# Kernel optimization log

Measured on AMD Instinct MI355X. Metric: run time of the kernel, lower is better.

Reference implementation:

```python
import jax, jax.numpy as jnp
import numpy as np

C = 64          # residual channels
N_LAYERS = 30
MAX_STEPS = 200
SQRT2 = 2.0 ** 0.5


def _conv1d(x, W, b, dilation=1, pad=0):
    # x: [B, Cin, T], W: [Cout, Cin, K], b: [Cout]
    y = jax.lax.conv_general_dilated(
        x, W, window_strides=(1,), padding=[(pad, pad)],
        rhs_dilation=(dilation,), dimension_numbers=('NCH', 'OIH', 'NCH'))
    return y + b[None, :, None]


def _silu(x):
    return x * jax.nn.sigmoid(x)


def _emb_table():
    steps = jnp.arange(MAX_STEPS, dtype=jnp.float32)[:, None]      # [200,1]
    dims = jnp.arange(64, dtype=jnp.float32)[None, :]              # [1,64]
    t = steps * 10.0 ** (dims * 4.0 / 63.0)                        # [200,64]
    return jnp.concatenate([jnp.sin(t), jnp.cos(t)], axis=1)       # [200,128]


def setup_inputs() -> dict:
    key = jax.random.key(0)
    ks = jax.random.split(key, 20)
    B, T = 4, 16384
    f32 = jnp.float32
    inp = {
        'audio': jax.random.normal(ks[0], (B, 1, T), dtype=f32),
        'diffusion_step': jax.random.randint(ks[1], (B,), 0, MAX_STEPS),
        # input projection Conv1d(1, 64, 1)
        'in_W': jax.random.normal(ks[2], (C, 1, 1), f32) * 1.0,
        'in_b': jax.random.normal(ks[3], (C,), f32) * 0.01,
        # diffusion embedding MLP 128->512->512
        'p1_W': jax.random.normal(ks[4], (512, 128), f32) * (1.0 / np.sqrt(128)),
        'p1_b': jnp.zeros((512,), f32),
        'p2_W': jax.random.normal(ks[5], (512, 512), f32) * (1.0 / np.sqrt(512)),
        'p2_b': jnp.zeros((512,), f32),
        # per-layer params (stacked over 30 layers)
        'dw_W': jax.random.normal(ks[6], (N_LAYERS, 2 * C, C, 3), f32) * (1.0 / np.sqrt(3 * C)),
        'dw_b': jnp.zeros((N_LAYERS, 2 * C), f32),
        'dp_W': jax.random.normal(ks[7], (N_LAYERS, C, 512), f32) * (1.0 / np.sqrt(512)),
        'dp_b': jnp.zeros((N_LAYERS, C), f32),
        'op_W': jax.random.normal(ks[8], (N_LAYERS, 2 * C, C, 1), f32) * (1.0 / np.sqrt(C)),
        'op_b': jnp.zeros((N_LAYERS, 2 * C), f32),
        # skip projection Conv1d(64,64,1)
        'sk_W': jax.random.normal(ks[9], (C, C, 1), f32) * (1.0 / np.sqrt(C)),
        'sk_b': jnp.zeros((C,), f32),
        # output projection Conv1d(64,1,1), weight zero-init like original
        'out_W': jnp.zeros((1, C, 1), f32),
        'out_b': jax.random.normal(ks[10], (1,), f32) * 0.01,
    }
    return inp


def reference(audio, diffusion_step, in_W, in_b, p1_W, p1_b, p2_W, p2_b,
              dw_W, dw_b, dp_W, dp_b, op_W, op_b, sk_W, sk_b, out_W, out_b):
    x = jax.nn.relu(_conv1d(audio, in_W, in_b))                    # [B,64,T]
    # diffusion embedding
    t = _emb_table()[diffusion_step]                               # [B,128]
    t = _silu(t @ p1_W.T + p1_b)                                   # [B,512]
    t = _silu(t @ p2_W.T + p2_b)                                   # [B,512]
    skip = None
    for i in range(N_LAYERS):
        d = 2 ** (i % 10)
        cond = (t @ dp_W[i].T + dp_b[i])[:, :, None]               # [B,64,1]
        y = _conv1d(x + cond, dw_W[i], dw_b[i], dilation=d, pad=d) # [B,128,T]
        gate, filt = y[:, :C], y[:, C:]
        y = jax.nn.sigmoid(gate) * jnp.tanh(filt)                  # [B,64,T]
        y = _conv1d(y, op_W[i], op_b[i])                           # [B,128,T]
        residual, sk = y[:, :C], y[:, C:]
        x = (x + residual) / SQRT2
        skip = sk if skip is None else skip + sk
    x = skip / np.sqrt(float(N_LAYERS)).astype(np.float32)
    x = jax.nn.relu(_conv1d(x, sk_W, sk_b))
    return _conv1d(x, out_W, out_b)                                # [B,1,T]
```

## Files before the change

kernel.cpp:

```cpp
#include <hip/hip_runtime.h>
#include <math.h>

#define C 64
#define NL 30
#define T 16384
#define B 4

typedef __bf16 bf16_t;
typedef __bf16 bf16x8 __attribute__((ext_vector_type(8)));
typedef __bf16 bf16x4 __attribute__((ext_vector_type(4)));
typedef float f32x4 __attribute__((ext_vector_type(4)));

typedef const __attribute__((address_space(1))) unsigned int glb_u32;
typedef __attribute__((address_space(3))) unsigned int lds_u32;

constexpr float INV_SQRT2   = 0.70710678118654752440f;
constexpr float INV_SQRT_NL = 0.18257418583505537115f;

__device__ __forceinline__ float fsig(float x) {
    return __builtin_amdgcn_rcpf(1.f + __builtin_amdgcn_exp2f(-1.44269504089f * x));
}
__device__ __forceinline__ float ftanh(float x) {
    return fmaf(2.f, __builtin_amdgcn_rcpf(1.f + __builtin_amdgcn_exp2f(-2.88539008178f * x)), -1.f);
}
// ... 37 lines not shown
    __syncthreads();
    int ol = tid >> 2, q = tid & 3;
    int o = blk * 64 + ol;
    const float4* wr = (const float4*)(p1_W + o * 128 + q * 32);
    const float4* ev = (const float4*)(e + q * 32);
    float a = 0.f;
    #pragma unroll
    for (int j = 0; j < 8; ++j) {
        float4 wv = wr[j]; float4 xv = ev[j];
        a = fmaf(wv.x, xv.x, a); a = fmaf(wv.y, xv.y, a);
        a = fmaf(wv.z, xv.z, a); a = fmaf(wv.w, xv.w, a);
    }
    red[tid] = a;
    __syncthreads();
    if (q == 0) {
        float v = red[tid] + red[tid + 1] + red[tid + 2] + red[tid + 3] + p1_b[o];
        h1out[b * 512 + o] = v / (1.f + expf(-v));
    }
}

__global__ void cond_p2(const float* __restrict__ h1,
                        const float* __restrict__ p2_W, const float* __restrict__ p2_b,
                        float* __restrict__ h2out) {
    __shared__ float red[256];
    int b = blockIdx.x, blk = blockIdx.y, tid = threadIdx.x;
    int ol = tid >> 2, q = tid & 3;
    int o = blk * 64 + ol;
    const float4* wr = (const float4*)(p2_W + o * 512 + q * 128);
    const float4* hv = (const float4*)(h1 + b * 512 + q * 128);
    float a = 0.f;
    #pragma unroll 8
    for (int j = 0; j < 32; ++j) {
        float4 wv = wr[j]; float4 xv = hv[j];
        a = fmaf(wv.x, xv.x, a); a = fmaf(wv.y, xv.y, a);
        a = fmaf(wv.z, xv.z, a); a = fmaf(wv.w, xv.w, a);
    }
    red[tid] = a;
    __syncthreads();
    if (q == 0) {
        float v = red[tid] + red[tid + 1] + red[tid + 2] + red[tid + 3] + p2_b[o];
        h2out[b * 512 + o] = v / (1.f + expf(-v));
    }
}

__global__ void cond_stage2b(const float* __restrict__ h2,
                             const float* __restrict__ dp_W, const float* __restrict__ dp_b,
                             const bf16_t* __restrict__ convpk,
                             const float* __restrict__ dw_b,
                             float* __restrict__ bias2) {
    __shared__ float red[256];
    __shared__ float cond_s[64];
    int l = blockIdx.x, b = blockIdx.y;
    int tid = threadIdx.x;
    {
        int o = tid >> 2, q = tid & 3;
        const float4* wr = (const float4*)(dp_W + ((size_t)l * C + o) * 512 + q * 128);
        const float4* h = (const float4*)(h2 + b * 512 + q * 128);
        float a = 0.f;
        #pragma unroll 8
        for (int j = 0; j < 32; ++j) {
            float4 wv = wr[j]; float4 hv = h[j];
            a = fmaf(wv.x, hv.x, a); a = fmaf(wv.y, hv.y, a);
            a = fmaf(wv.z, hv.z, a); a = fmaf(wv.w, hv.w, a);
        }
        red[tid] = a;
        __syncthreads();
        if (q == 0)
            cond_s[o] = red[tid] + red[tid + 1] + red[tid + 2] + red[tid + 3] + dp_b[l * C + o];
    }
    __syncthreads();
    int oc = tid & 127, kh = tid >> 7;
    const bf16_t* wr = convpk + ((size_t)l * 128 + oc) * 192 + kh * 96;
    float a = kh ? 0.f : dw_b[l * 128 + oc];
    #pragma unroll
    for (int j = 0; j < 96; ++j)
        a = fmaf((float)wr[j], cond_s[(kh * 96 + j) & 63], a);
    __syncthreads();
    red[tid] = a;
    __syncthreads();
    if (tid < 128)
        bias2[(l * B + b) * 128 + tid] = red[tid] + red[tid + 128];
}

__global__ __launch_bounds__(256, 4) void layer_kernel(
    const bf16_t* __restrict__ x_in, bf16_t* __restrict__ x_out, bf16_t* __restrict__ skip,
    const bf16_t* __restrict__ convpk, const bf16_t* __restrict__ oppk,
    const float* __restrict__ bias2, const float* __restrict__ op_b,
    const bf16_t* __restrict__ zpage,
    int layer, int dil, int first)
{
    __shared__ uint4 smem_u[2048];
    char* sm = (char*)smem_u;

    int tid = threadIdx.x;
    int w = __builtin_amdgcn_readfirstlane(tid >> 6);
    int l = tid & 63;
    int lr = l & 15;
    int g = l >> 4;
    int b = blockIdx.y;
    int bid = blockIdx.x;
    int tile = ((bid & 7) << 5) + (bid >> 3);
    int t0 = tile * 64;
    const bf16_t* xb = x_in + (size_t)b * T * 64;
    size_t bb = (size_t)b * T * 64;

    #pragma unroll
    for (int it = 0; it < 6; ++it) {
        int qq = it * 256 + tid;
        int slice = qq >> 9, row = (qq >> 3) & 63, c16 = qq & 7;
        int ts = t0 + row + (slice - 1) * dil;
        int c16s = c16 ^ (row & 7);
        const bf16_t* src = ((unsigned)ts < (unsigned)T)
            ? (xb + (size_t)ts * 64 + c16s * 8)
            : (zpage + c16s * 8);
        __builtin_amdgcn_global_load_lds((glb_u32*)src,
            (lds_u32*)(sm + it * 4096 + w * 1024), 16, 0, 0);
    }

    bf16x8 cA[2][6];
    const bf16_t* cw = convpk + (size_t)layer * 128 * 192;
    #pragma unroll
    for (int mf = 0; mf < 2; ++mf)
        #pragma unroll
        for (int kf = 0; kf < 6; ++kf)
            cA[mf][kf] = *(const bf16x8*)(cw + (mf * 64 + w * 16 + lr) * 192 + kf * 32 + g * 8);
    f32x4 bC[2];
    const float* b2 = bias2 + (layer * B + b) * 128;
    #pragma unroll
    for (int mf = 0; mf < 2; ++mf)
        #pragma unroll
        for (int r = 0; r < 4; ++r) bC[mf][r] = b2[mf * 64 + w * 16 + g * 4 + r];
    __syncthreads();

    f32x4 acc[2][4];
    #pragma unroll
    for (int mf = 0; mf < 2; ++mf)
        #pragma unroll
        for (int nf = 0; nf < 4; ++nf) acc[mf][nf] = bC[mf];
    #pragma unroll
    for (int kf = 0; kf < 6; ++kf) {
        int tap = kf >> 1;
        int kc = (kf & 1) * 32;
        bf16x8 Bf[4];
        #pragma unroll
        for (int nf = 0; nf < 4; ++nf) {
            int off = tap * 8192 + (nf * 16 + lr) * 128 + (kc + g * 8) * 2;
            Bf[nf] = *(const bf16x8*)(sm + swz(off));
        }
        #pragma unroll
        for (int mf = 0; mf < 2; ++mf)
            #pragma unroll
            for (int nf = 0; nf < 4; ++nf)
                acc[mf][nf] = __builtin_amdgcn_mfma_f32_16x16x32_bf16(
                    cA[mf][kf], Bf[nf], acc[mf][nf], 0, 0, 0);
    }

    bf16x8 oA[2][2];
    const bf16_t* ow = oppk + (size_t)layer * 128 * 64;
    #pragma unroll
    for (int mf = 0; mf < 2; ++mf)
        #pragma unroll
        for (int kf = 0; kf < 2; ++kf)
            oA[mf][kf] = *(const bf16x8*)(ow + (mf * 64 + w * 16 + lr) * 64 + kf * 32 + g * 8);
    f32x4 bO[2];
    const float* ob = op_b + layer * 2 * C;
    #pragma unroll
    for (int mf = 0; mf < 2; ++mf)
        #pragma unroll
        for (int r = 0; r < 4; ++r) bO[mf][r] = ob[mf * 64 + w * 16 + g * 4 + r];

    #pragma unroll
    for (int nf = 0; nf < 4; ++nf) {
        union { bf16_t hh[4]; uint2 u; } zp;
        #pragma unroll
        for (int r = 0; r < 4; ++r)
            zp.hh[r] = (bf16_t)(fsig(acc[0][nf][r]) * ftanh(acc[1][nf][r]));
        int off = 24576 + (nf * 16 + lr) * 128 + (w * 16 + g * 4) * 2;
        *(uint2*)(sm + swz(off)) = zp.u;
    }
    __syncthreads();

    f32x4 acc2[2][4];
    #pragma unroll
    for (int mf = 0; mf < 2; ++mf)
        #pragma unroll
        for (int nf = 0; nf < 4; ++nf) acc2[mf][nf] = bO[mf];
    #pragma unroll
    for (int kf = 0; kf < 2; ++kf) {
        bf16x8 Zf[4];
        #pragma unroll
        for (int nf = 0; nf < 4; ++nf) {
            int off = 24576 + (nf * 16 + lr) * 128 + (kf * 32 + g * 8) * 2;
            Zf[nf] = *(const bf16x8*)(sm + swz(off));
        }
        #pragma unroll
        for (int mf = 0; mf < 2; ++mf)
            #pragma unroll
            for (int nf = 0; nf < 4; ++nf)
                acc2[mf][nf] = __builtin_amdgcn_mfma_f32_16x16x32_bf16(
                    oA[mf][kf], Zf[nf], acc2[mf][nf], 0, 0, 0);
    }

    #pragma unroll
    for (int nf = 0; nf < 4; ++nf) {
        int t = t0 + nf * 16 + lr;
        int c0 = w * 16 + g * 4;
        int xoff = 8192 + (nf * 16 + lr) * 128 + c0 * 2;
        bf16x4 xv = *(const bf16x4*)(sm + swz(xoff));
        bf16x4 ro, so;
        bf16_t* sp = skip + bb + (size_t)t * 64 + c0;
        if (first) {
            #pragma unroll
            for (int r = 0; r < 4; ++r) {
                ro[r] = (bf16_t)(((float)xv[r] + acc2[0][nf][r]) * INV_SQRT2);
                so[r] = (bf16_t)acc2[1][nf][r];
            }
        } else {
            bf16x4 sv = *(const bf16x4*)sp;
            #pragma unroll
            for (int r = 0; r < 4; ++r) {
                ro[r] = (bf16_t)(((float)xv[r] + acc2[0][nf][r]) * INV_SQRT2);
                so[r] = (bf16_t)((float)sv[r] + acc2[1][nf][r]);
            }
        }
        *(bf16x4*)(x_out + bb + (size_t)t * 64 + c0) = ro;
        *(bf16x4*)sp = so;
    }
}

template<int D1, int D2, int YOFF, int NYR, int XOFF, int NXR, int FROMAUD>
__global__ __launch_bounds__(256) void fused_pair(
    const bf16_t* __restrict__ x_in, bf16_t* __restrict__ x_out,
    bf16_t* __restrict__ skip,
    const bf16_t* __restrict__ convpk, const bf16_t* __restrict__ oppk,
    const float* __restrict__ bias2, const float* __restrict__ op_b,
    const bf16_t* __restrict__ zpage,
    const float* __restrict__ audio,
    const float* __restrict__ in_W, const float* __restrict__ in_b,
    int layerA, int first)
{
    extern __shared__ char sm[];
    constexpr int NYF = NYR / 16;
    constexpr int CF  = YOFF / 16;
    constexpr int YS  = NXR * 128;
    constexpr int ZS  = YS + NYR * 128;

    int tid = threadIdx.x;
    int w = __builtin_amdgcn_readfirstlane(tid >> 6);
    int l = tid & 63, lr = l & 15, g = l >> 4;
    int bid = blockIdx.x;
    int tile = ((bid & 7) << 5) + (bid >> 3);
    int b = blockIdx.y;
    int t0 = tile * 64;
    size_t bb = (size_t)b * T * 64;
    const bf16_t* xb = x_in + bb;
    int c0 = w * 16 + g * 4;

    if constexpr (FROMAUD) {
        #pragma unroll
        for (int r = 0; r < NXR / 32; ++r) {
            int q = r * 256 + tid;
            int row = q >> 3, c16 = q & 7;
            int ts = t0 - XOFF + row;
            bf16x8 o;
            if ((unsigned)ts < (unsigned)T) {
                float av = audio[(size_t)b * T + ts];
                #pragma unroll
                for (int j = 0; j < 8; ++j) {
                    int c = c16 * 8 + j;
                    o[j] = (bf16_t)fmaxf(fmaf(in_W[c], av, in_b[c]), 0.f);
                }
            } else {
                #pragma unroll
                for (int j = 0; j < 8; ++j) o[j] = (bf16_t)0.f;
            }
            *(bf16x8*)(sm + swz(row * 128 + c16 * 16)) = o;
        }
    } else {
        #pragma unroll
        for (int r = 0; r < NXR / 32; ++r) {
            int row = r * 32 + (tid >> 3), c16 = tid & 7;
            int ts = t0 - XOFF + row;
            int c16s = c16 ^ (row & 7);
            const bf16_t* src = ((unsigned)ts < (unsigned)T)
                ? (xb + (size_t)ts * 64 + c16s * 8)
                : (zpage + c16s * 8);
            __builtin_amdgcn_global_load_lds((glb_u32*)src,
                (lds_u32*)(sm + r * 4096 + w * 1024), 16, 0, 0);
        }
    }

    float skr[16];
    #pragma unroll
    for (int i = 0; i < 16; ++i) skr[i] = 0.f;

    bf16x8 cA[2][6];
    {
        const bf16_t* cw = convpk + (size_t)layerA * 128 * 192;
        #pragma unroll
        for (int mf = 0; mf < 2; ++mf)
            #pragma unroll
            for (int kf = 0; kf < 6; ++kf)
                cA[mf][kf] = *(const bf16x8*)(cw + (mf * 64 + w * 16 + lr) * 192 + kf * 32 + g * 8);
    }
    bf16x8 oA[2][2];
    {
        const bf16_t* ow = oppk + (size_t)layerA * 128 * 64;
        #pragma unroll
        for (int mf = 0; mf < 2; ++mf)
            #pragma unroll
            for (int kf = 0; kf < 2; ++kf)
                oA[mf][kf] = *(const bf16x8*)(ow + (mf * 64 + w * 16 + lr) * 64 + kf * 32 + g * 8);
    }
    f32x4 bC[2], bO[2];
    {
        const float* b2 = bias2 + (layerA * B + b) * 128;
        const float* ob = op_b + layerA * 2 * C;
        #pragma unroll
        for (int mf = 0; mf < 2; ++mf)
            #pragma unroll
            for (int r = 0; r < 4; ++r) {
                bC[mf][r] = b2[mf * 64 + c0 + r];
                bO[mf][r] = ob[mf * 64 + c0 + r];
            }
    }
    __syncthreads();

    f32x4 acc[2][NYF];
    #pragma unroll
    for (int mf = 0; mf < 2; ++mf)
        #pragma unroll
        for (int nf = 0; nf < NYF; ++nf) acc[mf][nf] = bC[mf];
    #pragma unroll
    for (int kf = 0; kf < 6; ++kf) {
        int tap = kf >> 1;
        int kc = (kf & 1) * 32;
        bf16x8 Bf[NYF];
        #pragma unroll
        for (int nf = 0; nf < NYF; ++nf) {
            int ix = (nf * 16 + lr) + (XOFF - YOFF) + (tap - 1) * D1;
            Bf[nf] = *(const bf16x8*)(sm + swz(ix * 128 + (kc + g * 8) * 2));
        }
        #pragma unroll
        for (int mf = 0; mf < 2; ++mf)
            #pragma unroll
            for (int nf = 0; nf < NYF; ++nf)
                acc[mf][nf] = __builtin_amdgcn_mfma_f32_16x16x32_bf16(
                    cA[mf][kf], Bf[nf], acc[mf][nf], 0, 0, 0);
    }

    #pragma unroll
    for (int nf = 0; nf < NYF; ++nf) {
        union { bf16_t hh[4]; uint2 u; } zp;
        #pragma unroll
        for (int r = 0; r < 4; ++r)
            zp.hh[r] = (bf16_t)(fsig(acc[0][nf][r]) * ftanh(acc[1][nf][r]));
        int off = ZS + (nf * 16 + lr) * 128 + c0 * 2;
        *(uint2*)(sm + swz(off)) = zp.u;
    }
    __syncthreads();

    {
        f32x4 acc2[2][NYF];
        #pragma unroll
        for (int mf = 0; mf < 2; ++mf)
            #pragma unroll
            for (int nf = 0; nf < NYF; ++nf) acc2[mf][nf] = bO[mf];
        #pragma unroll
        for (int kf = 0; kf < 2; ++kf) {
            bf16x8 Zf[NYF];
            #pragma unroll
            for (int nf = 0; nf < NYF; ++nf) {
                int off = ZS + (nf * 16 + lr) * 128 + (kf * 32 + g * 8) * 2;
                Zf[nf] = *(const bf16x8*)(sm + swz(off));
            }
            #pragma unroll
            for (int mf = 0; mf < 2; ++mf)
                #pragma unroll
                for (int nf = 0; nf < NYF; ++nf)
                    acc2[mf][nf] = __builtin_amdgcn_mfma_f32_16x16x32_bf16(
                        oA[mf][kf], Zf[nf], acc2[mf][nf], 0, 0, 0);
        }
        #pragma unroll
        for (int nf = 0; nf < NYF; ++nf) {
            int iy = nf * 16 + lr;
            int ta = t0 - YOFF + iy;
            bool inr = ((unsigned)ta < (unsigned)T);
            int ixc = iy + (XOFF - YOFF);
            bf16x4 xv = *(const bf16x4*)(sm + swz(ixc * 128 + c0 * 2));
            bf16x4 yo;
            #pragma unroll
            for (int r = 0; r < 4; ++r) {
                float yv = ((float)xv[r] + acc2[0][nf][r]) * INV_SQRT2;
                yo[r] = inr ? (bf16_t)yv : (bf16_t)0.f;
                if (nf >= CF && nf < CF + 4)
                    skr[(nf - CF) * 4 + r] += acc2[1][nf][r];
            }
            *(bf16x4*)(sm + swz(YS + iy * 128 + c0 * 2)) = yo;
        }
    }

    int layerB = layerA + 1;
    bf16x8 cB[2][6];
    {
        const bf16_t* cw = convpk + (size_t)layerB * 128 * 192;
        #pragma unroll
        for (int mf = 0; mf < 2; ++mf)
            #pragma unroll
            for (int kf = 0; kf < 6; ++kf)
                cB[mf][kf] = *(const bf16x8*)(cw + (mf * 64 + w * 16 + lr) * 192 + kf * 32 + g * 8);
    }
    bf16x8 oB[2][2];
    {
        const bf16_t* ow = oppk + (size_t)layerB * 128 * 64;
        #pragma unroll
        for (int mf = 0; mf < 2; ++mf)
            #pragma unroll
            for (int kf = 0; kf < 2; ++kf)
                oB[mf][kf] = *(const bf16x8*)(ow + (mf * 64 + w * 16 + lr) * 64 + kf * 32 + g * 8);
    }
    f32x4 bCB[2], bOB[2];
    {
        const float* b2 = bias2 + (layerB * B + b) * 128;
        const float* ob = op_b + layerB * 2 * C;
        #pragma unroll
        for (int mf = 0; mf < 2; ++mf)
            #pragma unroll
            for (int r = 0; r < 4; ++r) {
                bCB[mf][r] = b2[mf * 64 + c0 + r];
                bOB[mf][r] = ob[mf * 64 + c0 + r];
            }
    }
    __syncthreads();

    f32x4 accB[2][4];
    #pragma unroll
    for (int mf = 0; mf < 2; ++mf)
        #pragma unroll
        for (int nf = 0; nf < 4; ++nf) accB[mf][nf] = bCB[mf];
    #pragma unroll
    for (int kf = 0; kf < 6; ++kf) {
        int tap = kf >> 1;
        int kc = (kf & 1) * 32;
        bf16x8 Bf[4];
        #pragma unroll
        for (int nf = 0; nf < 4; ++nf) {
            int jy = (nf * 16 + lr) + YOFF + (tap - 1) * D2;
            Bf[nf] = *(const bf16x8*)(sm + swz(YS + jy * 128 + (kc + g * 8) * 2));
        }
        #pragma unroll
        for (int mf = 0; mf < 2; ++mf)
            #pragma unroll
            for (int nf = 0; nf < 4; ++nf)
                accB[mf][nf] = __builtin_amdgcn_mfma_f32_16x16x32_bf16(
                    cB[mf][kf], Bf[nf], accB[mf][nf], 0, 0, 0);
    }

    #pragma unroll
    for (int nf = 0; nf < 4; ++nf) {
        union { bf16_t hh[4]; uint2 u; } zp;
        #pragma unroll
        for (int r = 0; r < 4; ++r)
            zp.hh[r] = (bf16_t)(fsig(accB[0][nf][r]) * ftanh(accB[1][nf][r]));
        int off = ZS + (nf * 16 + lr) * 128 + c0 * 2;
        *(uint2*)(sm + swz(off)) = zp.u;
    }
    __syncthreads();

    f32x4 acc2B[2][4];
    #pragma unroll
    for (int mf = 0; mf < 2; ++mf)
        #pragma unroll
        for (int nf = 0; nf < 4; ++nf) acc2B[mf][nf] = bOB[mf];
    #pragma unroll
    for (int kf = 0; kf < 2; ++kf) {
        bf16x8 Zf[4];
        #pragma unroll
        for (int nf = 0; nf < 4; ++nf) {
            int off = ZS + (nf * 16 + lr) * 128 + (kf * 32 + g * 8) * 2;
            Zf[nf] = *(const bf16x8*)(sm + swz(off));
        }
        #pragma unroll
        for (int mf = 0; mf < 2; ++mf)
            #pragma unroll
            for (int nf = 0; nf < 4; ++nf)
                acc2B[mf][nf] = __builtin_amdgcn_mfma_f32_16x16x32_bf16(
                    oB[mf][kf], Zf[nf], acc2B[mf][nf], 0, 0, 0);
    }
    #pragma unroll
    for (int nf = 0; nf < 4; ++nf) {
        int it = nf * 16 + lr;
        int t = t0 + it;
        int jyc = it + YOFF;
        bf16x4 yv = *(const bf16x4*)(sm + swz(YS + jyc * 128 + c0 * 2));
        bf16x4 ro, so;
        bf16_t* sp = skip + bb + (size_t)t * 64 + c0;
        if (first) {
            #pragma unroll
            for (int r = 0; r < 4; ++r) {
                ro[r] = (bf16_t)(((float)yv[r] + acc2B[0][nf][r]) * INV_SQRT2);
                so[r] = (bf16_t)(skr[nf * 4 + r] + acc2B[1][nf][r]);
            }
        } else {
            bf16x4 sv = *(const bf16x4*)sp;
            #pragma unroll
            for (int r = 0; r < 4; ++r) {
                ro[r] = (bf16_t)(((float)yv[r] + acc2B[0][nf][r]) * INV_SQRT2);
                so[r] = (bf16_t)((float)sv[r] + skr[nf * 4 + r] + acc2B[1][nf][r]);
            }
        }
        *(bf16x4*)(x_out + bb + (size_t)t * 64 + c0) = ro;
        *(bf16x4*)sp = so;
    }
}

__global__ __launch_bounds__(256) void final_kernel(
    const bf16_t* __restrict__ skip, const bf16_t* __restrict__ skpk,
    const float* __restrict__ sk_b,
    const float* __restrict__ out_W, const float* __restrict__ out_b,
    float* __restrict__ out)
{
    __shared__ uint4 tile_u[512];
    __shared__ float part[16][66];
    unsigned char* sm = (unsigned char*)tile_u;
    int tid = threadIdx.x;
    int w = __builtin_amdgcn_readfirstlane(tid >> 6);
    int l = tid & 63, lr = l & 15, g = l >> 4;
    int bid = blockIdx.x;
    int tile = ((bid & 7) << 5) + (bid >> 3);
    int b = blockIdx.y, t0 = tile * 64;
    const bf16_t* sb = skip + (size_t)b * T * 64;

    #pragma unroll
    for (int it = 0; it < 2; ++it) {
        int q = it * 256 + tid;
        int row = q >> 3, c16 = q & 7;
        uint4 val = *(const uint4*)(sb + (size_t)(t0 + row) * 64 + c16 * 8);
        *(uint4*)(sm + swz(row * 128 + c16 * 16)) = val;
    }

    bf16x8 aS[2];
    #pragma unroll
    for (int kf = 0; kf < 2; ++kf)
        aS[kf] = *(const bf16x8*)(skpk + (w * 16 + lr) * 64 + kf * 32 + g * 8);
    f32x4 acc[4];
    #pragma unroll
    for (int nf = 0; nf < 4; ++nf)
        #pragma unroll
        for (int r = 0; r < 4; ++r) acc[nf][r] = sk_b[w * 16 + g * 4 + r];
    __syncthreads();

    #pragma unroll
    for (int kf = 0; kf < 2; ++kf) {
        bf16x8 Bf[4];
        #pragma unroll
        for (int nf = 0; nf < 4; ++nf) {
            int off = (nf * 16 + lr) * 128 + (kf * 32 + g * 8) * 2;
            Bf[nf] = *(const bf16x8*)(sm + swz(off));
        }
        #pragma unroll
        for (int nf = 0; nf < 4; ++nf)
            acc[nf] = __builtin_amdgcn_mfma_f32_16x16x32_bf16(aS[kf], Bf[nf], acc[nf], 0, 0, 0);
    }

    #pragma unroll
    for (int nf = 0; nf < 4; ++nf) {
        float o = 0.f;
        #pragma unroll
        for (int r = 0; r < 4; ++r)
            o = fmaf(out_W[w * 16 + g * 4 + r], fmaxf(acc[nf][r], 0.f), o);
        part[w * 4 + g][nf * 16 + lr] = o;
    }
    __syncthreads();
    if (tid < 64) {
        float o = out_b[0];
        #pragma unroll
        for (int j = 0; j < 16; ++j) o += part[j][tid];
        out[(size_t)b * T + t0 + tid] = o;
    }
}

extern "C" void kernel_launch(void* const* d_in, const int* in_sizes, int n_in,
                              void* d_out, int out_size, void* d_ws, size_t ws_size,
                              hipStream_t stream) {
    const float* audio = (const float*)d_in[0];
    const int*   dstep = (const int*)d_in[1];
    const float* in_W  = (const float*)d_in[2];
    const float* in_b  = (const float*)d_in[3];
    const float* p1_W  = (const float*)d_in[4];
    const float* p1_b  = (const float*)d_in[5];
    const float* p2_W  = (const float*)d_in[6];
    const float* p2_b  = (const float*)d_in[7];
    const float* dw_W  = (const float*)d_in[8];
    const float* dw_b  = (const float*)d_in[9];
    const float* dp_W  = (const float*)d_in[10];
    const float* dp_b  = (const float*)d_in[11];
    const float* op_W  = (const float*)d_in[12];
    const float* op_b  = (const float*)d_in[13];
    const float* sk_W  = (const float*)d_in[14];
    const float* sk_b  = (const float*)d_in[15];
    const float* out_W = (const float*)d_in[16];
    const float* out_b = (const float*)d_in[17];

    float* ws = (float*)d_ws;
    const size_t NXE = (size_t)B * T * 64;
    float* h1    = ws;
    float* h2    = h1 + B * 512;
    float* bias2 = h2 + B * 512;
    float* zpg   = bias2 + NL * B * 128;
    bf16_t* xA   = (bf16_t*)(zpg + 128);
    bf16_t* xB   = xA + NXE;
    bf16_t* skip = xB + NXE;
    bf16_t* convpk = skip + NXE;
    bf16_t* oppk   = convpk + (size_t)NL * 128 * 192;
    bf16_t* skpk   = oppk + (size_t)NL * 128 * 64;

    hipMemsetAsync(zpg, 0, 512, stream);
    hipLaunchKernelGGL(pack_weights, dim3(3856), dim3(256), 0, stream,
                       dw_W, op_W, sk_W, convpk, oppk, skpk);
    hipLaunchKernelGGL(cond_embp1, dim3(B, 8), dim3(256), 0, stream,
                       dstep, p1_W, p1_b, h1);
    hipLaunchKernelGGL(cond_p2, dim3(B, 8), dim3(256), 0, stream,
                       h1, p2_W, p2_b, h2);
    hipLaunchKernelGGL(cond_stage2b, dim3(NL, B), dim3(256), 0, stream,
                       h2, dp_W, dp_b, convpk, dw_b, bias2);

    bf16_t* bufs[2] = { xA, xB };
    int cur = 0;
    const bf16_t* zpgc = (const bf16_t*)zpg;
    for (int dec = 0; dec < 3; ++dec) {
        int base = dec * 10;
        if (dec == 0) {
            hipLaunchKernelGGL((fused_pair<1, 2, 16, 96, 32, 128, 1>),
                               dim3(T / 64, B), dim3(256), 40960, stream,
                               bufs[cur], bufs[cur ^ 1], skip, convpk, oppk,
                               bias2, op_b, zpgc, audio, in_W, in_b, 0, 1);
        } else {
            hipLaunchKernelGGL((fused_pair<1, 2, 16, 96, 32, 128, 0>),
                               dim3(T / 64, B), dim3(256), 40960, stream,
                               bufs[cur], bufs[cur ^ 1], skip, convpk, oppk,
                               bias2, op_b, zpgc, audio, in_W, in_b, base + 0, 0);
        }
        cur ^= 1;
        hipLaunchKernelGGL((fused_pair<4, 8, 16, 96, 32, 128, 0>),
                           dim3(T / 64, B), dim3(256), 40960, stream,
                           bufs[cur], bufs[cur ^ 1], skip, convpk, oppk,
                           bias2, op_b, zpgc, audio, in_W, in_b, base + 2, 0);
        cur ^= 1;
        hipLaunchKernelGGL((fused_pair<16, 32, 32, 128, 48, 160, 0>),
                           dim3(T / 64, B), dim3(256), 53248, stream,
                           bufs[cur], bufs[cur ^ 1], skip, convpk, oppk,
                           bias2, op_b, zpgc, audio, in_W, in_b, base + 4, 0);
        cur ^= 1;
        for (int j = 6; j < 10; ++j) {
            int dil = 1 << j;
            hipLaunchKernelGGL(layer_kernel, dim3(T / 64, B), dim3(256), 0, stream,
                               bufs[cur], bufs[cur ^ 1], skip, convpk, oppk,
                               bias2, op_b, zpgc, base + j, dil, 0);
            cur ^= 1;
        }
    }
    hipLaunchKernelGGL(final_kernel, dim3(T / 64, B), dim3(256), 0, stream,
                       skip, skpk, sk_b, out_W, out_b, (float*)d_out);
}
```

Before: 484.9 us.

## Fuse three dilated layers per kernel and process two tiles per block in layer_kernel

Result: slower. 519.2 us (+7.1%).

```diff
diff --git a/kernel.cpp b/kernel.cpp
--- a/kernel.cpp
+++ b/kernel.cpp
@@ -143,7 +143,7 @@
         bias2[(l * B + b) * 128 + tid] = red[tid] + red[tid + 128];
 }
 
-__global__ __launch_bounds__(256, 4) void layer_kernel(
+__global__ __launch_bounds__(256) void layer_kernel(
     const bf16_t* __restrict__ x_in, bf16_t* __restrict__ x_out, bf16_t* __restrict__ skip,
     const bf16_t* __restrict__ convpk, const bf16_t* __restrict__ oppk,
     const float* __restrict__ bias2, const float* __restrict__ op_b,
@@ -160,23 +160,9 @@
     int g = l >> 4;
     int b = blockIdx.y;
     int bid = blockIdx.x;
-    int tile = ((bid & 7) << 5) + (bid >> 3);
-    int t0 = tile * 64;
+    int tile = ((bid & 7) << 4) + (bid >> 3);
+    int tbase = tile * 128;
     const bf16_t* xb = x_in + (size_t)b * T * 64;
-    size_t bb = (size_t)b * T * 64;
-
-    #pragma unroll
-    for (int it = 0; it < 6; ++it) {
-        int qq = it * 256 + tid;
-        int slice = qq >> 9, row = (qq >> 3) & 63, c16 = qq & 7;
-        int ts = t0 + row + (slice - 1) * dil;
-        int c16s = c16 ^ (row & 7);
-        const bf16_t* src = ((unsigned)ts < (unsigned)T)
-            ? (xb + (size_t)ts * 64 + c16s * 8)
-            : (zpage + c16s * 8);
-        __builtin_amdgcn_global_load_lds((glb_u32*)src,
-            (lds_u32*)(sm + it * 4096 + w * 1024), 16, 0, 0);
-    }
 
     bf16x8 cA[2][6];
     const bf16_t* cw = convpk + (size_t)layer * 128 * 192;
@@ -185,37 +171,6 @@
         #pragma unroll
         for (int kf = 0; kf < 6; ++kf)
             cA[mf][kf] = *(const bf16x8*)(cw + (mf * 64 + w * 16 + lr) * 192 + kf * 32 + g * 8);
-    f32x4 bC[2];
-    const float* b2 = bias2 + (layer * B + b) * 128;
-    #pragma unroll
-    for (int mf = 0; mf < 2; ++mf)
-        #pragma unroll
-        for (int r = 0; r < 4; ++r) bC[mf][r] = b2[mf * 64 + w * 16 + g * 4 + r];
-    __syncthreads();
-
-    f32x4 acc[2][4];
-    #pragma unroll
-    for (int mf = 0; mf < 2; ++mf)
-        #pragma unroll
-        for (int nf = 0; nf < 4; ++nf) acc[mf][nf] = bC[mf];
-    #pragma unroll
-    for (int kf = 0; kf < 6; ++kf) {
-        int tap = kf >> 1;
-        int kc = (kf & 1) * 32;
-        bf16x8 Bf[4];
-        #pragma unroll
-        for (int nf = 0; nf < 4; ++nf) {
-            int off = tap * 8192 + (nf * 16 + lr) * 128 + (kc + g * 8) * 2;
-            Bf[nf] = *(const bf16x8*)(sm + swz(off));
-        }
-        #pragma unroll
-        for (int mf = 0; mf < 2; ++mf)
-            #pragma unroll
-            for (int nf = 0; nf < 4; ++nf)
-                acc[mf][nf] = __builtin_amdgcn_mfma_f32_16x16x32_bf16(
-                    cA[mf][kf], Bf[nf], acc[mf][nf], 0, 0, 0);
-    }
-
     bf16x8 oA[2][2];
     const bf16_t* ow = oppk + (size_t)layer * 128 * 64;
     #pragma unroll
@@ -223,74 +178,123 @@
         #pragma unroll
         for (int kf = 0; kf < 2; ++kf)
             oA[mf][kf] = *(const bf16x8*)(ow + (mf * 64 + w * 16 + lr) * 64 + kf * 32 + g * 8);
-    f32x4 bO[2];
+    f32x4 bC[2], bO[2];
+    const float* b2 = bias2 + (layer * B + b) * 128;
     const float* ob = op_b + layer * 2 * C;
     #pragma unroll
     for (int mf = 0; mf < 2; ++mf)
         #pragma unroll
-        for (int r = 0; r < 4; ++r) bO[mf][r] = ob[mf * 64 + w * 16 + g * 4 + r];
-
-    #pragma unroll
-    for (int nf = 0; nf < 4; ++nf) {
-        union { bf16_t hh[4]; uint2 u; } zp;
-        #pragma unroll
-        for (int r = 0; r < 4; ++r)
-            zp.hh[r] = (bf16_t)(fsig(acc[0][nf][r]) * ftanh(acc[1][nf][r]));
-        int off = 24576 + (nf * 16 + lr) * 128 + (w * 16 + g * 4) * 2;
-        *(uint2*)(sm + swz(off)) = zp.u;
-    }
-    __syncthreads();
-
-    f32x4 acc2[2][4];
-    #pragma unroll
-    for (int mf = 0; mf < 2; ++mf)
-        #pragma unroll
-        for (int nf = 0; nf < 4; ++nf) acc2[mf][nf] = bO[mf];
-    #pragma unroll
-    for (int kf = 0; kf < 2; ++kf) {
-        bf16x8 Zf[4];
+        for (int r = 0; r < 4; ++r) {
+            bC[mf][r] = b2[mf * 64 + w * 16 + g * 4 + r];
+            bO[mf][r] = ob[mf * 64 + w * 16 + g * 4 + r];
+        }
+
+    size_t bb = (size_t)b * T * 64;
+
+    for (int st = 0; st < 2; ++st) {
+        int t0 = tbase + st * 64;
+
+        #pragma unroll
+        for (int it = 0; it < 6; ++it) {
+            int qq = it * 256 + tid;
+            int slice = qq >> 9, row = (qq >> 3) & 63, c16 = qq & 7;
+            int ts = t0 + row + (slice - 1) * dil;
+            int c16s = c16 ^ (row & 7);
+            const bf16_t* src = ((unsigned)ts < (unsigned)T)
+                ? (xb + (size_t)ts * 64 + c16s * 8)
+                : (zpage + c16s * 8);
+            __builtin_amdgcn_global_load_lds((glb_u32*)src,
+                (lds_u32*)(sm + it * 4096 + w * 1024), 16, 0, 0);
+        }
+        __syncthreads();
+
+        f32x4 acc[2][4];
+        #pragma unroll
+        for (int mf = 0; mf < 2; ++mf)
+            #pragma unroll
+            for (int nf = 0; nf < 4; ++nf) acc[mf][nf] = bC[mf];
+        #pragma unroll
+        for (int kf = 0; kf < 6; ++kf) {
+            int tap = kf >> 1;
+            int kc = (kf & 1) * 32;
+            bf16x8 Bf[4];
+            #pragma unroll
+            for (int nf = 0; nf < 4; ++nf) {
+                int off = tap * 8192 + (nf * 16 + lr) * 128 + (kc + g * 8) * 2;
+                Bf[nf] = *(const bf16x8*)(sm + swz(off));
+            }
+            #pragma unroll
+            for (int mf = 0; mf < 2; ++mf)
+                #pragma unroll
+                for (int nf = 0; nf < 4; ++nf)
+                    acc[mf][nf] = __builtin_amdgcn_mfma_f32_16x16x32_bf16(
+                        cA[mf][kf], Bf[nf], acc[mf][nf], 0, 0, 0);
+        }
+
         #pragma unroll
         for (int nf = 0; nf < 4; ++nf) {
-            int off = 24576 + (nf * 16 + lr) * 128 + (kf * 32 + g * 8) * 2;
-            Zf[nf] = *(const bf16x8*)(sm + swz(off));
-        }
+            union { bf16_t hh[4]; uint2 u; } zp;
+            #pragma unroll
+            for (int r = 0; r < 4; ++r)
+                zp.hh[r] = (bf16_t)(fsig(acc[0][nf][r]) * ftanh(acc[1][nf][r]));
+            int off = 24576 + (nf * 16 + lr) * 128 + (w * 16 + g * 4) * 2;
+            *(uint2*)(sm + swz(off)) = zp.u;
+        }
+        __syncthreads();
+
+        f32x4 acc2[2][4];
         #pragma unroll
         for (int mf = 0; mf < 2; ++mf)
             #pragma unroll
-            for (int nf = 0; nf < 4; ++nf)
-                acc2[mf][nf] = __builtin_amdgcn_mfma_f32_16x16x32_bf16(
-                    oA[mf][kf], Zf[nf], acc2[mf][nf], 0, 0, 0);
-    }
-
-    #pragma unroll
-    for (int nf = 0; nf < 4; ++nf) {
-        int t = t0 + nf * 16 + lr;
-        int c0 = w * 16 + g * 4;
-        int xoff = 8192 + (nf * 16 + lr) * 128 + c0 * 2;
-        bf16x4 xv = *(const bf16x4*)(sm + swz(xoff));
-        bf16x4 ro, so;
-        bf16_t* sp = skip + bb + (size_t)t * 64 + c0;
-        if (first) {
-            #pragma unroll
-            for (int r = 0; r < 4; ++r) {
-                ro[r] = (bf16_t)(((float)xv[r] + acc2[0][nf][r]) * INV_SQRT2);
-                so[r] = (bf16_t)acc2[1][nf][r];
-            }
-        } else {
-            bf16x4 sv = *(const bf16x4*)sp;
-            #pragma unroll
-            for (int r = 0; r < 4; ++r) {
-                ro[r] = (bf16_t)(((float)xv[r] + acc2[0][nf][r]) * INV_SQRT2);
-                so[r] = (bf16_t)((float)sv[r] + acc2[1][nf][r]);
-            }
-        }
-        *(bf16x4*)(x_out + bb + (size_t)t * 64 + c0) = ro;
-        *(bf16x4*)sp = so;
-    }
-}
-
-template<int D1, int D2, int YOFF, int NYR, int XOFF, int NXR, int FROMAUD>
-__global__ __launch_bounds__(256) void fused_pair(
+            for (int nf = 0; nf < 4; ++nf) acc2[mf][nf] = bO[mf];
+        #pragma unroll
+        for (int kf = 0; kf < 2; ++kf) {
+            bf16x8 Zf[4];
+            #pragma unroll
+            for (int nf = 0; nf < 4; ++nf) {
+                int off = 24576 + (nf * 16 + lr) * 128 + (kf * 32 + g * 8) * 2;
+                Zf[nf] = *(const bf16x8*)(sm + swz(off));
+            }
+            #pragma unroll
+            for (int mf = 0; mf < 2; ++mf)
+                #pragma unroll
+                for (int nf = 0; nf < 4; ++nf)
+                    acc2[mf][nf] = __builtin_amdgcn_mfma_f32_16x16x32_bf16(
+                        oA[mf][kf], Zf[nf], acc2[mf][nf], 0, 0, 0);
+        }
+
+        #pragma unroll
+        for (int nf = 0; nf < 4; ++nf) {
+            int t = t0 + nf * 16 + lr;
+            int c0 = w * 16 + g * 4;
+            int xoff = 8192 + (nf * 16 + lr) * 128 + c0 * 2;
+            bf16x4 xv = *(const bf16x4*)(sm + swz(xoff));
+            bf16x4 ro, so;
+            bf16_t* sp = skip + bb + (size_t)t * 64 + c0;
+            if (first) {
+                #pragma unroll
+                for (int r = 0; r < 4; ++r) {
+                    ro[r] = (bf16_t)(((float)xv[r] + acc2[0][nf][r]) * INV_SQRT2);
+                    so[r] = (bf16_t)acc2[1][nf][r];
+                }
+            } else {
+                bf16x4 sv = *(const bf16x4*)sp;
+                #pragma unroll
+                for (int r = 0; r < 4; ++r) {
+                    ro[r] = (bf16_t)(((float)xv[r] + acc2[0][nf][r]) * INV_SQRT2);
+                    so[r] = (bf16_t)((float)sv[r] + acc2[1][nf][r]);
+                }
+            }
+            *(bf16x4*)(x_out + bb + (size_t)t * 64 + c0) = ro;
+            *(bf16x4*)sp = so;
+        }
+        if (st == 0) __syncthreads();
+    }
+}
+
+template<int D1, int D2, int D3, int YB, int NYB, int YA, int NYA,
+         int XO, int NXR, int FROMAUD>
+__global__ __launch_bounds__(256) void fused_triple(
     const bf16_t* __restrict__ x_in, bf16_t* __restrict__ x_out,
     bf16_t* __restrict__ skip,
     const bf16_t* __restrict__ convpk, const bf16_t* __restrict__ oppk,
@@ -301,10 +305,12 @@
     int layerA, int first)
 {
     extern __shared__ char sm[];
-    constexpr int NYF = NYR / 16;
-    constexpr int CF  = YOFF / 16;
+    constexpr int NAF = NYA / 16;
+    constexpr int NBF = NYB / 16;
+    constexpr int CFA = YA / 16;
+    constexpr int CFB = YB / 16;
     constexpr int YS  = NXR * 128;
-    constexpr int ZS  = YS + NYR * 128;
+    constexpr int ZS  = YS + NYA * 128;
 
     int tid = threadIdx.x;
     int w = __builtin_amdgcn_readfirstlane(tid >> 6);
@@ -322,7 +328,7 @@
         for (int r = 0; r < NXR / 32; ++r) {
             int q = r * 256 + tid;
             int row = q >> 3, c16 = q & 7;
-            int ts = t0 - XOFF + row;
+            int ts = t0 - XO + row;
             bf16x8 o;
             if ((unsigned)ts < (unsigned)T) {
                 float av = audio[(size_t)b * T + ts];
@@ -341,7 +347,7 @@
         #pragma unroll
         for (int r = 0; r < NXR / 32; ++r) {
             int row = r * 32 + (tid >> 3), c16 = tid & 7;
-            int ts = t0 - XOFF + row;
+            int ts = t0 - XO + row;
             int c16s = c16 ^ (row & 7);
             const bf16_t* src = ((unsigned)ts < (unsigned)T)
                 ? (xb + (size_t)ts * 64 + c16s * 8)
@@ -355,223 +361,296 @@
     #pragma unroll
     for (int i = 0; i < 16; ++i) skr[i] = 0.f;
 
-    bf16x8 cA[2][6];
+    bf16x8 cW[2][6], oW[2][2];
+    f32x4 bC[2], bO[2];
     {
         const bf16_t* cw = convpk + (size_t)layerA * 128 * 192;
-        #pragma unroll
-        for (int mf = 0; mf < 2; ++mf)
-            #pragma unroll
-            for (int kf = 0; kf < 6; ++kf)
-                cA[mf][kf] = *(const bf16x8*)(cw + (mf * 64 + w * 16 + lr) * 192 + kf * 32 + g * 8);
-    }
-    bf16x8 oA[2][2];
-    {
         const bf16_t* ow = oppk + (size_t)layerA * 128 * 64;
-        #pragma unroll
-        for (int mf = 0; mf < 2; ++mf)
-            #pragma unroll
-            for (int kf = 0; kf < 2; ++kf)
-                oA[mf][kf] = *(const bf16x8*)(ow + (mf * 64 + w * 16 + lr) * 64 + kf * 32 + g * 8);
-    }
-    f32x4 bC[2], bO[2];
-    {
         const float* b2 = bias2 + (layerA * B + b) * 128;
         const float* ob = op_b + layerA * 2 * C;
         #pragma unroll
-        for (int mf = 0; mf < 2; ++mf)
+        for (int mf = 0; mf < 2; ++mf) {
+            #pragma unroll
+            for (int kf = 0; kf < 6; ++kf)
+                cW[mf][kf] = *(const bf16x8*)(cw + (mf * 64 + w * 16 + lr) * 192 + kf * 32 + g * 8);
+            #pragma unroll
+            for (int kf = 0; kf < 2; ++kf)
+                oW[mf][kf] = *(const bf16x8*)(ow + (mf * 64 + w * 16 + lr) * 64 + kf * 32 + g * 8);
             #pragma unroll
             for (int r = 0; r < 4; ++r) {
                 bC[mf][r] = b2[mf * 64 + c0 + r];
                 bO[mf][r] = ob[mf * 64 + c0 + r];
             }
-    }
-    __syncthreads();
-
-    f32x4 acc[2][NYF];
-    #pragma unroll
-    for (int mf = 0; mf < 2; ++mf)
-        #pragma unroll
-        for (int nf = 0; nf < NYF; ++nf) acc[mf][nf] = bC[mf];
-    #pragma unroll
-    for (int kf = 0; kf < 6; ++kf) {
-        int tap = kf >> 1;
-        int kc = (kf & 1) * 32;
-        bf16x8 Bf[NYF];
-        #pragma unroll
-        for (int nf = 0; nf < NYF; ++nf) {
-            int ix = (nf * 16 + lr) + (XOFF - YOFF) + (tap - 1) * D1;
-            Bf[nf] = *(const bf16x8*)(sm + swz(ix * 128 + (kc + g * 8) * 2));
-        }
+        }
+    }
+    __syncthreads();
+
+    {
+        f32x4 acc[2][NAF];
         #pragma unroll
         for (int mf = 0; mf < 2; ++mf)
             #pragma unroll
-            for (int nf = 0; nf < NYF; ++nf)
-                acc[mf][nf] = __builtin_amdgcn_mfma_f32_16x16x32_bf16(
-                    cA[mf][kf], Bf[nf], acc[mf][nf], 0, 0, 0);
-    }
-
-    #pragma unroll
-    for (int nf = 0; nf < NYF; ++nf) {
-        union { bf16_t hh[4]; uint2 u; } zp;
-        #pragma unroll
-        for (int r = 0; r < 4; ++r)
-            zp.hh[r] = (bf16_t)(fsig(acc[0][nf][r]) * ftanh(acc[1][nf][r]));
-        int off = ZS + (nf * 16 + lr) * 128 + c0 * 2;
-        *(uint2*)(sm + swz(off)) = zp.u;
-    }
-    __syncthreads();
-
-    {
-        f32x4 acc2[2][NYF];
+            for (int nf = 0; nf < NAF; ++nf) acc[mf][nf] = bC[mf];
+        #pragma unroll
+        for (int kf = 0; kf < 6; ++kf) {
+            int tap = kf >> 1;
+            int kc = (kf & 1) * 32;
+            bf16x8 Bf[NAF];
+            #pragma unroll
+            for (int nf = 0; nf < NAF; ++nf) {
+                int ix = (nf * 16 + lr) + (XO - YA) + (tap - 1) * D1;
+                Bf[nf] = *(const bf16x8*)(sm + swz(ix * 128 + (kc + g * 8) * 2));
+            }
+            #pragma unroll
+            for (int mf = 0; mf < 2; ++mf)
+                #pragma unroll
+                for (int nf = 0; nf < NAF; ++nf)
+                    acc[mf][nf] = __builtin_amdgcn_mfma_f32_16x16x32_bf16(
+                        cW[mf][kf], Bf[nf], acc[mf][nf], 0, 0, 0);
+        }
+        #pragma unroll
+        for (int nf = 0; nf < NAF; ++nf) {
+            union { bf16_t hh[4]; uint2 u; } zp;
+            #pragma unroll
+            for (int r = 0; r < 4; ++r)
+                zp.hh[r] = (bf16_t)(fsig(acc[0][nf][r]) * ftanh(acc[1][nf][r]));
+            *(uint2*)(sm + swz(ZS + (nf * 16 + lr) * 128 + c0 * 2)) = zp.u;
+        }
+    }
+    __syncthreads();
+
+    {
+        f32x4 acc2[2][NAF];
         #pragma unroll
         for (int mf = 0; mf < 2; ++mf)
             #pragma unroll
-            for (int nf = 0; nf < NYF; ++nf) acc2[mf][nf] = bO[mf];
+            for (int nf = 0; nf < NAF; ++nf) acc2[mf][nf] = bO[mf];
         #pragma unroll
         for (int kf = 0; kf < 2; ++kf) {
-            bf16x8 Zf[NYF];
-            #pragma unroll
-            for (int nf = 0; nf < NYF; ++nf) {
-                int off = ZS + (nf * 16 + lr) * 128 + (kf * 32 + g * 8) * 2;
-                Zf[nf] = *(const bf16x8*)(sm + swz(off));
-            }
+            bf16x8 Zf[NAF];
+            #pragma unroll
+            for (int nf = 0; nf < NAF; ++nf)
+                Zf[nf] = *(const bf16x8*)(sm + swz(ZS + (nf * 16 + lr) * 128 + (kf * 32 + g * 8) * 2));
             #pragma unroll
             for (int mf = 0; mf < 2; ++mf)
                 #pragma unroll
-                for (int nf = 0; nf < NYF; ++nf)
+                for (int nf = 0; nf < NAF; ++nf)
                     acc2[mf][nf] = __builtin_amdgcn_mfma_f32_16x16x32_bf16(
-                        oA[mf][kf], Zf[nf], acc2[mf][nf], 0, 0, 0);
-        }
-        #pragma unroll
-        for (int nf = 0; nf < NYF; ++nf) {
+                        oW[mf][kf], Zf[nf], acc2[mf][nf], 0, 0, 0);
+        }
+        #pragma unroll
+        for (int nf = 0; nf < NAF; ++nf) {
             int iy = nf * 16 + lr;
-            int ta = t0 - YOFF + iy;
+            int ta = t0 - YA + iy;
             bool inr = ((unsigned)ta < (unsigned)T);
-            int ixc = iy + (XOFF - YOFF);
+            int ixc = iy + (XO - YA);
             bf16x4 xv = *(const bf16x4*)(sm + swz(ixc * 128 + c0 * 2));
             bf16x4 yo;
             #pragma unroll
             for (int r = 0; r < 4; ++r) {
                 float yv = ((float)xv[r] + acc2[0][nf][r]) * INV_SQRT2;
                 yo[r] = inr ? (bf16_t)yv : (bf16_t)0.f;
-                if (nf >= CF && nf < CF + 4)
-                    skr[(nf - CF) * 4 + r] += acc2[1][nf][r];
+                if (nf >= CFA && nf < CFA + 4)
+                    skr[(nf - CFA) * 4 + r] += acc2[1][nf][r];
             }
             *(bf16x4*)(sm + swz(YS + iy * 128 + c0 * 2)) = yo;
         }
     }
-
-    int layerB = layerA + 1;
-    bf16x8 cB[2][6];
-    {
+    {
+        int layerB = layerA + 1;
         const bf16_t* cw = convpk + (size_t)layerB * 128 * 192;
-        #pragma unroll
-        for (int mf = 0; mf < 2; ++mf)
-            #pragma unroll
-            for (int kf = 0; kf < 6; ++kf)
-                cB[mf][kf] = *(const bf16x8*)(cw + (mf * 64 + w * 16 + lr) * 192 + kf * 32 + g * 8);
-    }
-    bf16x8 oB[2][2];
-    {
         const bf16_t* ow = oppk + (size_t)layerB * 128 * 64;
-        #pragma unroll
-        for (int mf = 0; mf < 2; ++mf)
-            #pragma unroll
-            for (int kf = 0; kf < 2; ++kf)
-                oB[mf][kf] = *(const bf16x8*)(ow + (mf * 64 + w * 16 + lr) * 64 + kf * 32 + g * 8);
-    }
-    f32x4 bCB[2], bOB[2];
-    {
         const float* b2 = bias2 + (layerB * B + b) * 128;
         const float* ob = op_b + layerB * 2 * C;
         #pragma unroll
+        for (int mf = 0; mf < 2; ++mf) {
+            #pragma unroll
+            for (int kf = 0; kf < 6; ++kf)
+                cW[mf][kf] = *(const bf16x8*)(cw + (mf * 64 + w * 16 + lr) * 192 + kf * 32 + g * 8);
+            #pragma unroll
+            for (int kf = 0; kf < 2; ++kf)
+                oW[mf][kf] = *(const bf16x8*)(ow + (mf * 64 + w * 16 + lr) * 64 + kf * 32 + g * 8);
+            #pragma unroll
+            for (int r = 0; r < 4; ++r) {
+                bC[mf][r] = b2[mf * 64 + c0 + r];
+                bO[mf][r] = ob[mf * 64 + c0 + r];
+            }
+        }
+    }
+    __syncthreads();
+
+    {
+        f32x4 acc[2][NBF];
+        #pragma unroll
         for (int mf = 0; mf < 2; ++mf)
             #pragma unroll
+            for (int nf = 0; nf < NBF; ++nf) acc[mf][nf] = bC[mf];
+        #pragma unroll
+        for (int kf = 0; kf < 6; ++kf) {
+            int tap = kf >> 1;
+            int kc = (kf & 1) * 32;
+            bf16x8 Bf[NBF];
+            #pragma unroll
+            for (int nf = 0; nf < NBF; ++nf) {
+                int jy = (nf * 16 + lr) + (YA - YB) + (tap - 1) * D2;
+                Bf[nf] = *(const bf16x8*)(sm + swz(YS + jy * 128 + (kc + g * 8) * 2));
+            }
+            #pragma unroll
+            for (int mf = 0; mf < 2; ++mf)
+                #pragma unroll
+                for (int nf = 0; nf < NBF; ++nf)
+                    acc[mf][nf] = __builtin_amdgcn_mfma_f32_16x16x32_bf16(
+                        cW[mf][kf], Bf[nf], acc[mf][nf], 0, 0, 0);
+        }
+        #pragma unroll
+        for (int nf = 0; nf < NBF; ++nf) {
+            union { bf16_t hh[4]; uint2 u; } zp;
+            #pragma unroll
+            for (int r = 0; r < 4; ++r)
+                zp.hh[r] = (bf16_t)(fsig(acc[0][nf][r]) * ftanh(acc[1][nf][r]));
+            *(uint2*)(sm + swz(ZS + (nf * 16 + lr) * 128 + c0 * 2)) = zp.u;
+        }
+    }
+    __syncthreads();
+
+    {
+        f32x4 acc2[2][NBF];
+        #pragma unroll
+        for (int mf = 0; mf < 2; ++mf)
+            #pragma unroll
+            for (int nf = 0; nf < NBF; ++nf) acc2[mf][nf] = bO[mf];
+        #pragma unroll
+        for (int kf = 0; kf < 2; ++kf) {
+            bf16x8 Zf[NBF];
+            #pragma unroll
+            for (int nf = 0; nf < NBF; ++nf)
+                Zf[nf] = *(const bf16x8*)(sm + swz(ZS + (nf * 16 + lr) * 128 + (kf * 32 + g * 8) * 2));
+            #pragma unroll
+            for (int mf = 0; mf < 2; ++mf)
+                #pragma unroll
+                for (int nf = 0; nf < NBF; ++nf)
+                    acc2[mf][nf] = __builtin_amdgcn_mfma_f32_16x16x32_bf16(
+                        oW[mf][kf], Zf[nf], acc2[mf][nf], 0, 0, 0);
+        }
+        #pragma unroll
+        for (int nf = 0; nf < NBF; ++nf) {
+            int k = nf * 16 + lr;
+            int tb2 = t0 - YB + k;
+            bool inr = ((unsigned)tb2 < (unsigned)T);
+            int jyc = k + (YA - YB);
+            bf16x4 yv = *(const bf16x4*)(sm + swz(YS + jyc * 128 + c0 * 2));
+            bf16x4 yo;
+            #pragma unroll
             for (int r = 0; r < 4; ++r) {
-                bCB[mf][r] = b2[mf * 64 + c0 + r];
-                bOB[mf][r] = ob[mf * 64 + c0 + r];
-            }
-    }
-    __syncthreads();
-
-    f32x4 accB[2][4];
-    #pragma unroll
-    for (int mf = 0; mf < 2; ++mf)
-        #pragma unroll
-        for (int nf = 0; nf < 4; ++nf) accB[mf][nf] = bCB[mf];
-    #pragma unroll
-    for (int kf = 0; kf < 6; ++kf) {
-        int tap = kf >> 1;
-        int kc = (kf & 1) * 32;
-        bf16x8 Bf[4];
+                float vv = ((float)yv[r] + acc2[0][nf][r]) * INV_SQRT2;
+                yo[r] = inr ? (bf16_t)vv : (bf16_t)0.f;
+                if (nf >= CFB && nf < CFB + 4)
+                    skr[(nf - CFB) * 4 + r] += acc2[1][nf][r];
+            }
+            *(bf16x4*)(sm + swz(k * 128 + c0 * 2)) = yo;
+        }
+    }
+    {
+        int layerC = layerA + 2;
+        const bf16_t* cw = convpk + (size_t)layerC * 128 * 192;
+        const bf16_t* ow = oppk + (size_t)layerC * 128 * 64;
+        const float* b2 = bias2 + (layerC * B + b) * 128;
+        const float* ob = op_b + layerC * 2 * C;
+        #pragma unroll
+        for (int mf = 0; mf < 2; ++mf) {
+            #pragma unroll
+            for (int kf = 0; kf < 6; ++kf)
+                cW[mf][kf] = *(const bf16x8*)(cw + (mf * 64 + w * 16 + lr) * 192 + kf * 32 + g * 8);
+            #pragma unroll
+            for (int kf = 0; kf < 2; ++kf)
+                oW[mf][kf] = *(const bf16x8*)(ow + (mf * 64 + w * 16 + lr) * 64 + kf * 32 + g * 8);
+            #pragma unroll
+            for (int r = 0; r < 4; ++r) {
+                bC[mf][r] = b2[mf * 64 + c0 + r];
+                bO[mf][r] = ob[mf * 64 + c0 + r];
+            }
+        }
+    }
+    __syncthreads();
+
+    {
+        f32x4 acc[2][4];
+        #pragma unroll
+        for (int mf = 0; mf < 2; ++mf)
+            #pragma unroll
+            for (int nf = 0; nf < 4; ++nf) acc[mf][nf] = bC[mf];
+        #pragma unroll
+        for (int kf = 0; kf < 6; ++kf) {
+            int tap = kf >> 1;
+            int kc = (kf & 1) * 32;
+            bf16x8 Bf[4];
+            #pragma unroll
+            for (int nf = 0; nf < 4; ++nf) {
+                int ky = (nf * 16 + lr) + YB + (tap - 1) * D3;
+                Bf[nf] = *(const bf16x8*)(sm + swz(ky * 128 + (kc + g * 8) * 2));
+            }
+            #pragma unroll
+            for (int mf = 0; mf < 2; ++mf)
+                #pragma unroll
+                for (int nf = 0; nf < 4; ++nf)
+                    acc[mf][nf] = __builtin_amdgcn_mfma_f32_16x16x32_bf16(
+                        cW[mf][kf], Bf[nf], acc[mf][nf], 0, 0, 0);
+        }
         #pragma unroll
         for (int nf = 0; nf < 4; ++nf) {
-            int jy = (nf * 16 + lr) + YOFF + (tap - 1) * D2;
-            Bf[nf] = *(const bf16x8*)(sm + swz(YS + jy * 128 + (kc + g * 8) * 2));
-        }
+            union { bf16_t hh[4]; uint2 u; } zp;
+            #pragma unroll
+            for (int r = 0; r < 4; ++r)
+                zp.hh[r] = (bf16_t)(fsig(acc[0][nf][r]) * ftanh(acc[1][nf][r]));
+            *(uint2*)(sm + swz(ZS + (nf * 16 + lr) * 128 + c0 * 2)) = zp.u;
+        }
+    }
+    __syncthreads();
+
+    {
+        f32x4 acc2[2][4];
         #pragma unroll
         for (int mf = 0; mf < 2; ++mf)
             #pragma unroll
+            for (int nf = 0; nf < 4; ++nf) acc2[mf][nf] = bO[mf];
+        #pragma unroll
+        for (int kf = 0; kf < 2; ++kf) {
+            bf16x8 Zf[4];
+            #pragma unroll
             for (int nf = 0; nf < 4; ++nf)
-                accB[mf][nf] = __builtin_amdgcn_mfma_f32_16x16x32_bf16(
-                    cB[mf][kf], Bf[nf], accB[mf][nf], 0, 0, 0);
-    }
-
-    #pragma unroll
-    for (int nf = 0; nf < 4; ++nf) {
-        union { bf16_t hh[4]; uint2 u; } zp;
-        #pragma unroll
-        for (int r = 0; r < 4; ++r)
-            zp.hh[r] = (bf16_t)(fsig(accB[0][nf][r]) * ftanh(accB[1][nf][r]));
-        int off = ZS + (nf * 16 + lr) * 128 + c0 * 2;
-        *(uint2*)(sm + swz(off)) = zp.u;
-    }
-    __syncthreads();
-
-    f32x4 acc2B[2][4];
-    #pragma unroll
-    for (int mf = 0; mf < 2; ++mf)
-        #pragma unroll
-        for (int nf = 0; nf < 4; ++nf) acc2B[mf][nf] = bOB[mf];
-    #pragma unroll
-    for (int kf = 0; kf < 2; ++kf) {
-        bf16x8 Zf[4];
+                Zf[nf] = *(const bf16x8*)(sm + swz(ZS + (nf * 16 + lr) * 128 + (kf * 32 + g * 8) * 2));
+            #pragma unroll
+            for (int mf = 0; mf < 2; ++mf)
+                #pragma unroll
+                for (int nf = 0; nf < 4; ++nf)
+                    acc2[mf][nf] = __builtin_amdgcn_mfma_f32_16x16x32_bf16(
+                        oW[mf][kf], Zf[nf], acc2[mf][nf], 0, 0, 0);
+        }
         #pragma unroll
         for (int nf = 0; nf < 4; ++nf) {
-            int off = ZS + (nf * 16 + lr) * 128 + (kf * 32 + g * 8) * 2;
-            Zf[nf] = *(const bf16x8*)(sm + swz(off));
-        }
-        #pragma unroll
-        for (int mf = 0; mf < 2; ++mf)
-            #pragma unroll
-            for (int nf = 0; nf < 4; ++nf)
-                acc2B[mf][nf] = __builtin_amdgcn_mfma_f32_16x16x32_bf16(
-                    oB[mf][kf], Zf[nf], acc2B[mf][nf], 0, 0, 0);
-    }
-    #pragma unroll
-    for (int nf = 0; nf < 4; ++nf) {
-        int it = nf * 16 + lr;
-        int t = t0 + it;
-        int jyc = it + YOFF;
-        bf16x4 yv = *(const bf16x4*)(sm + swz(YS + jyc * 128 + c0 * 2));
-        bf16x4 ro, so;
-        bf16_t* sp = skip + bb + (size_t)t * 64 + c0;
-        if (first) {
-            #pragma unroll
-            for (int r = 0; r < 4; ++r) {
-                ro[r] = (bf16_t)(((float)yv[r] + acc2B[0][nf][r]) * INV_SQRT2);
-                so[r] = (bf16_t)(skr[nf * 4 + r] + acc2B[1][nf][r]);
-            }
-        } else {
-            bf16x4 sv = *(const bf16x4*)sp;
-            #pragma unroll
-            for (int r = 0; r < 4; ++r) {
-                ro[r] = (bf16_t)(((float)yv[r] + acc2B[0][nf][r]) * INV_SQRT2);
-                so[r] = (bf16_t)((float)sv[r] + skr[nf * 4 + r] + acc2B[1][nf][r]);
-            }
-        }
-        *(bf16x4*)(x_out + bb + (size_t)t * 64 + c0) = ro;
-        *(bf16x4*)sp = so;
+            int it = nf * 16 + lr;
+            int t = t0 + it;
+            int kyc = it + YB;
+            bf16x4 yv = *(const bf16x4*)(sm + swz(kyc * 128 + c0 * 2));
+            bf16x4 ro, so;
+            bf16_t* sp = skip + bb + (size_t)t * 64 + c0;
+            if (first) {
+                #pragma unroll
+                for (int r = 0; r < 4; ++r) {
+                    ro[r] = (bf16_t)(((float)yv[r] + acc2[0][nf][r]) * INV_SQRT2);
+                    so[r] = (bf16_t)(skr[nf * 4 + r] + acc2[1][nf][r]);
+                }
+            } else {
+                bf16x4 sv = *(const bf16x4*)sp;
+                #pragma unroll
+                for (int r = 0; r < 4; ++r) {
+                    ro[r] = (bf16_t)(((float)yv[r] + acc2[0][nf][r]) * INV_SQRT2);
+                    so[r] = (bf16_t)((float)sv[r] + skr[nf * 4 + r] + acc2[1][nf][r]);
+                }
+            }
+            *(bf16x4*)(x_out + bb + (size_t)t * 64 + c0) = ro;
+            *(bf16x4*)sp = so;
+        }
     }
 }
 
@@ -692,35 +771,30 @@
     for (int dec = 0; dec < 3; ++dec) {
         int base = dec * 10;
         if (dec == 0) {
-            hipLaunchKernelGGL((fused_pair<1, 2, 16, 96, 32, 128, 1>),
-                               dim3(T / 64, B), dim3(256), 40960, stream,
+            hipLaunchKernelGGL((fused_triple<1, 2, 4, 16, 96, 32, 128, 48, 160, 1>),
+                               dim3(256, B), dim3(256), 53248, stream,
                                bufs[cur], bufs[cur ^ 1], skip, convpk, oppk,
                                bias2, op_b, zpgc, audio, in_W, in_b, 0, 1);
         } else {
-            hipLaunchKernelGGL((fused_pair<1, 2, 16, 96, 32, 128, 0>),
-                               dim3(T / 64, B), dim3(256), 40960, stream,
+            hipLaunchKernelGGL((fused_triple<1, 2, 4, 16, 96, 32, 128, 48, 160, 0>),
+                               dim3(256, B), dim3(256), 53248, stream,
                                bufs[cur], bufs[cur ^ 1], skip, convpk, oppk,
                                bias2, op_b, zpgc, audio, in_W, in_b, base + 0, 0);
         }
         cur ^= 1;
-        hipLaunchKernelGGL((fused_pair<4, 8, 16, 96, 32, 128, 0>),
-                           dim3(T / 64, B), dim3(256), 40960, stream,
+        hipLaunchKernelGGL((fused_triple<8, 16, 32, 32, 128, 48, 160, 64, 192, 0>),
+                           dim3(256, B), dim3(256), 65536, stream,
                            bufs[cur], bufs[cur ^ 1], skip, convpk, oppk,
-                           bias2, op_b, zpgc, audio, in_W, in_b, base + 2, 0);
-        cur ^= 1;
-        hipLaunchKernelGGL((fused_pair<16, 32, 32, 128, 48, 160, 0>),
-                           dim3(T / 64, B), dim3(256), 53248, stream,
-                           bufs[cur], bufs[cur ^ 1], skip, convpk, oppk,
-                           bias2, op_b, zpgc, audio, in_W, in_b, base + 4, 0);
+                           bias2, op_b, zpgc, audio, in_W, in_b, base + 3, 0);
         cur ^= 1;
         for (int j = 6; j < 10; ++j) {
             int dil = 1 << j;
-            hipLaunchKernelGGL(layer_kernel, dim3(T / 64, B), dim3(256), 0, stream,
+            hipLaunchKernelGGL(layer_kernel, dim3(T / 128, B), dim3(256), 0, stream,
                                bufs[cur], bufs[cur ^ 1], skip, convpk, oppk,
                                bias2, op_b, zpgc, base + j, dil, 0);
             cur ^= 1;
         }
     }
-    hipLaunchKernelGGL(final_kernel, dim3(T / 64, B), dim3(256), 0, stream,
+    hipLaunchKernelGGL(final_kernel, dim3(256, B), dim3(256), 0, stream,
                        skip, skpk, sk_b, out_W, out_b, (float*)d_out);
 }
```
